# Kernel tuning notes

Measured on AMD Instinct MI355X. Metric: run time of the kernel, lower is better.

The kernel has to match this reference:

```python
import jax, jax.numpy as jnp
import numpy as np

DIM, HEADS, DHEAD = 256, 8, 64
INNER = HEADS * DHEAD
EPS = 1e-5


def _ln(x, g, b):
    m = x.mean(-1, keepdims=True)
    v = ((x - m) ** 2).mean(-1, keepdims=True)
    return (x - m) / jnp.sqrt(v + EPS) * g + b


def setup_inputs() -> dict:
    key = jax.random.key(0)
    ks = jax.random.split(key, 24)
    b, n, Q, K = 1, 6, 900, 1408
    d = DIM
    s = lambda fan_in: 1.0 / np.sqrt(fan_in)
    inp = {
        "k_g": jax.random.normal(ks[0], (b, n, K, d), jnp.float32),
        "q_g": jax.random.normal(ks[1], (b, n, Q, d), jnp.float32),
        "k_a": jax.random.normal(ks[2], (b, n, K, d), jnp.float32),
        "q_a": jax.random.normal(ks[3], (b, Q, d), jnp.float32),
        "v": jax.random.normal(ks[4], (b, n, K, d), jnp.float32),
        "mask": jax.random.randint(ks[5], (b, n, K), 0, 2).astype(bool),
        # projections (stored as (in, out))
        "W_qg": jax.random.uniform(ks[6], (d, INNER), jnp.float32, -s(d), s(d)),
        "b_qg": jnp.zeros((INNER,), jnp.float32),
        "W_kg": jax.random.uniform(ks[7], (d, INNER), jnp.float32, -s(d), s(d)),
        "b_kg": jnp.zeros((INNER,), jnp.float32),
        "W_qa": jax.random.uniform(ks[8], (d, INNER), jnp.float32, -s(d), s(d)),
        "b_qa": jnp.zeros((INNER,), jnp.float32),
        "W_ka": jax.random.uniform(ks[9], (d, INNER), jnp.float32, -s(d), s(d)),
        "b_ka": jnp.zeros((INNER,), jnp.float32),
        "W_v": jax.random.uniform(ks[10], (d, INNER), jnp.float32, -s(d), s(d)),
        "b_v": jnp.zeros((INNER,), jnp.float32),
        "W_o": jax.random.uniform(ks[11], (INNER, d), jnp.float32, -s(INNER), s(INNER)),
        "b_o": jnp.zeros((d,), jnp.float32),
        "ln1_g": jnp.ones((d,), jnp.float32),
        "ln1_b": jnp.zeros((d,), jnp.float32),
        "W_m1": jax.random.uniform(ks[12], (d, 2 * d), jnp.float32, -s(d), s(d)),
        "b_m1": jnp.zeros((2 * d,), jnp.float32),
        "W_m2": jax.random.uniform(ks[13], (2 * d, d), jnp.float32, -s(2 * d), s(2 * d)),
        "b_m2": jnp.zeros((d,), jnp.float32),
        "ln2_g": jnp.ones((d,), jnp.float32),
        "ln2_b": jnp.zeros((d,), jnp.float32),
        "scale_g": jnp.full((HEADS,), DHEAD ** -0.5, jnp.float32),
        "scale_a": jnp.full((HEADS,), DHEAD ** -0.5, jnp.float32),
    }
    return inp


def reference(k_g, q_g, k_a, q_a, v, mask,
              W_qg, b_qg, W_kg, b_kg, W_qa, b_qa, W_ka, b_ka, W_v, b_v,
              W_o, b_o, ln1_g, ln1_b, W_m1, b_m1, W_m2, b_m2, ln2_g, ln2_b,
              scale_g, scale_a):
    b, n, Q, _ = q_g.shape
    K = k_g.shape[2]
    h, dh = HEADS, DHEAD
    skip = q_a

    def split(x):  # (..., h*dh) -> (b, h, ..., dh)
        return jnp.moveaxis(x.reshape(x.shape[:-1] + (h, dh)), -2, 1)

    kg = split(k_g @ W_kg + b_kg)          # (b, h, n, K, dh)
    qg = split(q_g @ W_qg + b_qg)          # (b, h, n, Q, dh)
    ka = split(k_a @ W_ka + b_ka)          # (b, h, n, K, dh)
    qa = split(q_a @ W_qa + b_qa)          # (b, h, Q, dh)
    vv = split(v @ W_v + b_v)              # (b, h, n, K, dh)

    dot_g = jnp.einsum('bhnqd,bhnkd->bhnqk', qg, kg)
    dot_a = jnp.einsum('bhqd,bhnkd->bhnqk', qa, ka)
    sg = scale_g[None, :, None, None, None]
    sa = scale_a[None, :, None, None, None]
    dot = sg * dot_g + sa * dot_a
    dot = jnp.where(mask[:, None, :, None, :], -jnp.inf, dot)

    # softmax jointly over (n, K)
    dot = dot.transpose(0, 1, 3, 2, 4).reshape(b, h, Q, n * K)
    att = jax.nn.softmax(dot, axis=-1)
    vflat = vv.reshape(b, h, n * K, dh)
    a = jnp.einsum('bhqk,bhkd->bhqd', att, vflat)
    a = a.transpose(0, 2, 1, 3).reshape(b, Q, h * dh)

    z = a @ W_o + b_o + skip
    z = _ln(z, ln1_g, ln1_b)
    z = z + (jax.nn.gelu(z @ W_m1 + b_m1, approximate=False) @ W_m2 + b_m2)
    z = _ln(z, ln2_g, ln2_b)
    return z
```

## Files before the change

kernel.cpp:

```cpp
#include <hip/hip_runtime.h>
#include <stdint.h>

typedef unsigned short u16;
typedef _Float16 half8 __attribute__((ext_vector_type(8)));
typedef _Float16 half4 __attribute__((ext_vector_type(4)));
typedef _Float16 half2 __attribute__((ext_vector_type(2)));
typedef float f32x4 __attribute__((ext_vector_type(4)));

__device__ __forceinline__ u16 f2h(float f) {
    _Float16 h = (_Float16)f; u16 u; __builtin_memcpy(&u, &h, 2); return u;
}
__device__ __forceinline__ float h2f(u16 u) {
    _Float16 h; __builtin_memcpy(&h, &u, 2); return (float)h;
}

template<int CTRL>
__device__ __forceinline__ float dppf(float x) {
    return __builtin_bit_cast(float,
        __builtin_amdgcn_update_dpp(0, __builtin_bit_cast(int, x), CTRL, 0xF, 0xF, false));
}
__device__ __forceinline__ float sum16(float x) {
    x += dppf<0xB1>(x);
    x += dppf<0x4E>(x);
    x += dppf<0x124>(x);
    x += dppf<0x128>(x);
    return x;
}

__global__ __launch_bounds__(256) void prep_kernel(
    const float* __restrict__ W_qg, const float* __restrict__ W_kg,
    const float* __restrict__ W_qa, const float* __restrict__ W_ka,
    const float* __restrict__ W_v,  const float* __restrict__ W_o,
    const float* __restrict__ W_m1, const float* __restrict__ W_m2,
    u16* __restrict__ T_qg, u16* __restrict__ T_kg, u16* __restrict__ T_qa,
    u16* __restrict__ T_ka, u16* __restrict__ T_v,  u16* __restrict__ T_o,
    u16* __restrict__ T_m1, u16* __restrict__ T_m2,
    const float* __restrict__ scale_g, const float* __restrict__ scale_a,
    const float* __restrict__ b_kg, const float* __restrict__ b_ka,
    float* __restrict__ bkg_s, float* __restrict__ bka_s,
    const int* __restrict__ mask, int* __restrict__ mflag)
{
    const int z = blockIdx.z;
    const int tid = threadIdx.x;
    if (z == 8) {
        if (blockIdx.y != 0) return;
        if (blockIdx.x == 0) {
            __shared__ int f;
            if (tid == 0) f = 0;
            __syncthreads();
            int local = 0;
            for (int i = tid; i < 2112; i += 256) { int vv = mask[i]; if (vv & ~1) local = 1; }
            if (local) atomicOr(&f, 1);
            __syncthreads();
            if (tid == 0) *mflag = f;
        } else if (blockIdx.x == 1) {
            for (int j = tid; j < 512; j += 256) {
                bkg_s[j] = b_kg[j] * scale_g[j >> 6];
                bka_s[j] = b_ka[j] * scale_a[j >> 6];
            }
        }
        return;
    }
    const int K = (z == 5 || z == 7) ? 512 : 256;
    const int N = (z == 5 || z == 7) ? 256 : 512;
    const int k0 = blockIdx.x * 64, n0 = blockIdx.y * 64;
    if (k0 >= K || n0 >= N) return;
    const float* W = z==0?W_qg: z==1?W_kg: z==2?W_qa: z==3?W_ka: z==4?W_v: z==5?W_o: z==6?W_m1: W_m2;
    u16* D        = z==0?T_qg: z==1?T_kg: z==2?T_qa: z==3?T_ka: z==4?T_v: z==5?T_o: z==6?T_m1: T_m2;
    const float* scp = z==1 ? scale_g : z==3 ? scale_a : nullptr;

    __shared__ u16 T[64][80];
    const int cr = tid >> 4, cc = (tid & 15) * 4;
    const float sc = scp ? scp[(n0 + cc) >> 6] : 1.0f;
    #pragma unroll
    for (int i = 0; i < 4; ++i) {
        const int r = cr + i * 16;
        const float4 vv = *(const float4*)(W + (size_t)(k0 + r) * N + n0 + cc);
        T[cc + 0][r] = f2h(vv.x * sc);
        T[cc + 1][r] = f2h(vv.y * sc);
        T[cc + 2][r] = f2h(vv.z * sc);
        T[cc + 3][r] = f2h(vv.w * sc);
    }
    __syncthreads();
    const int nr = tid >> 2, part = (tid & 3) * 16;
    u16* drow = D + (size_t)(n0 + nr) * K + k0 + part;
    *(half8*)(drow)     = *(const half8*)&T[nr][part];
    *(half8*)(drow + 8) = *(const half8*)&T[nr][part + 8];
}

__global__ __launch_bounds__(256, 4) void proj_all(
    const float* __restrict__ k_g, const float* __restrict__ k_a,
    const float* __restrict__ v,   const float* __restrict__ q_g,
    const float* __restrict__ q_a,
    const u16* __restrict__ T_kg, const u16* __restrict__ T_ka,
    const u16* __restrict__ T_v,  const u16* __restrict__ T_qg,
    const u16* __restrict__ T_qa,
    const float* __restrict__ bkg_s, const float* __restrict__ bka_s,
    const float* __restrict__ b_v,   const float* __restrict__ b_qg,
    const float* __restrict__ b_qa,
    u16* __restrict__ qcat, u16* __restrict__ kcat, u16* __restrict__ vt)
{
    __shared__ u16 Ws[256 * 36];

    int bx = blockIdx.x;
    int mode, M;
    const float* X; const u16* Wt; const float* bias; u16* out;
    if (bx < 132)      { mode = 2; M = 8448; X = k_g; Wt = T_kg; bias = bkg_s; out = kcat; }
    else if (bx < 264) { mode = 3; M = 8448; X = k_a; Wt = T_ka; bias = bka_s; out = kcat; bx -= 132; }
    else if (bx < 396) { mode = 4; M = 8448; X = v;   Wt = T_v;  bias = b_v;   out = vt;   bx -= 264; }
    else if (bx < 481) { mode = 0; M = 5400; X = q_g; Wt = T_qg; bias = b_qg;  out = qcat; bx -= 396; }
    else               { mode = 1; M = 900;  X = q_a; Wt = T_qa; bias = b_qa;  out = qcat; bx -= 481; }
    const int rows_per_n = (mode == 0) ? 900 : 1408;

    const int tid = threadIdx.x;
    const int w = tid >> 6, lane = tid & 63;
    const int l15 = lane & 15, quad = lane >> 4;
    const int m0 = bx * 64;
    const int nbase = blockIdx.y * 256;
    const int row = m0 + w * 16 + l15;

    const float* xrow = X + (size_t)(row < M ? row : 0) * 256 + quad * 8;
    const u16* wcol = Wt + ((size_t)(nbase + tid) << 8);

    f32x4 o[4][4];
    #pragma unroll
    for (int nt = 0; nt < 4; ++nt)
        #pragma unroll
        for (int t = 0; t < 4; ++t) { o[nt][t][0]=0.f; o[nt][t][1]=0.f; o[nt][t][2]=0.f; o[nt][t][3]=0.f; }

    for (int k0 = 0; k0 < 8; ++k0) {
        {
            const uint4 w0 = *(const uint4*)(wcol + k0 * 32 + 0);
            const uint4 w1 = *(const uint4*)(wcol + k0 * 32 + 8);
            const uint4 w2 = *(const uint4*)(wcol + k0 * 32 + 16);
            const uint4 w3 = *(const uint4*)(wcol + k0 * 32 + 24);
            *(uint4*)&Ws[tid * 36 + 0]  = w0;
            *(uint4*)&Ws[tid * 36 + 8]  = w1;
            *(uint4*)&Ws[tid * 36 + 16] = w2;
            *(uint4*)&Ws[tid * 36 + 24] = w3;
        }
        __syncthreads();

        const float4 a0 = *(const float4*)(xrow + k0 * 32);
        const float4 a1 = *(const float4*)(xrow + k0 * 32 + 4);
        half8 af;
        af[0]=(_Float16)a0.x; af[1]=(_Float16)a0.y; af[2]=(_Float16)a0.z; af[3]=(_Float16)a0.w;
        af[4]=(_Float16)a1.x; af[5]=(_Float16)a1.y; af[6]=(_Float16)a1.z; af[7]=(_Float16)a1.w;

        #pragma unroll
        for (int nt = 0; nt < 4; ++nt)
            #pragma unroll
            for (int t = 0; t < 4; ++t) {
                const half8 bf = *(const half8*)&Ws[(nt * 64 + t * 16 + l15) * 36 + quad * 8];
                o[nt][t] = __builtin_amdgcn_mfma_f32_16x16x32_f16(af, bf, o[nt][t], 0, 0, 0);
            }
        __syncthreads();
    }

    #pragma unroll
    for (int nt = 0; nt < 4; ++nt) {
        const int n0 = nbase + nt * 64;
        const int hh = n0 >> 6;
        float bj[4];
        #pragma unroll
        for (int t = 0; t < 4; ++t) bj[t] = bias[n0 + t * 16 + l15];

        if (mode == 4) {
            const int gr0 = m0 + w * 16 + quad * 4;
            if (gr0 < M) {
                const int nI = gr0 / rows_per_n;
                const int rr = gr0 - nI * rows_per_n;
                u16* vb = out + (size_t)(hh * 6 + nI) * 64 * 1408;
                #pragma unroll
                for (int t = 0; t < 4; ++t) {
                    const int d = t * 16 + l15;
                    ushort4 pk;
                    pk.x = f2h(o[nt][t][0] + bj[t]);
                    pk.y = f2h(o[nt][t][1] + bj[t]);
                    pk.z = f2h(o[nt][t][2] + bj[t]);
                    pk.w = f2h(o[nt][t][3] + bj[t]);
                    *(ushort4*)&vb[(size_t)d * 1408 + rr] = pk;
                }
            }
        } else if (mode == 1) {
            #pragma unroll
            for (int r = 0; r < 4; ++r) {
                const int gr = m0 + w * 16 + quad * 4 + r;
                if (gr < M) {
                    for (int nb = 0; nb < 6; ++nb) {
                        u16* qb = out + (((size_t)(hh * 6 + nb) * 900 + gr) << 7) + 64;
                        #pragma unroll
                        for (int t = 0; t < 4; ++t)
                            qb[t * 16 + l15] = f2h(o[nt][t][r] + bj[t]);
                    }
                }
            }
        } else {
            const size_t kdim = (mode == 0) ? 900 : 1408;
            const int doff = (mode == 3) ? 64 : 0;
            #pragma unroll
            for (int r = 0; r < 4; ++r) {
                const int gr = m0 + w * 16 + quad * 4 + r;
                if (gr < M) {
                    const int nI = gr / rows_per_n;
                    const int rr = gr - nI * rows_per_n;
                    u16* ob = out + (((size_t)(hh * 6 + nI) * kdim + rr) << 7) + doff;
                    #pragma unroll
                    for (int t = 0; t < 4; ++t)
                        ob[t * 16 + l15] = f2h(o[nt][t][r] + bj[t]);
                }
            }
        }
    }
}

__global__ __launch_bounds__(512, 4) void attn_kernel(
    const u16* __restrict__ qcat, const u16* __restrict__ kcat,
    const u16* __restrict__ vt, const void* __restrict__ maskp,
    const int* __restrict__ mflag,
    u16* __restrict__ Opart, float* __restrict__ lpart)
{
    __shared__ __align__(16) u16 Ks[64 * 136];
    __shared__ __align__(16) u16 Vs[64 * 72];
    __shared__ __align__(16) u16 Ps[8][1216];
    __shared__ float Mb[64];

    const int flat = blockIdx.x;
    const int hn_i = (flat & 7) + 8 * ((flat >> 3) % 6);
    const int rest = flat / 48;
    const int qt = rest & 7;
    const int sp = rest >> 3;
    const int n = hn_i - (hn_i / 6) * 6;

    const int q0 = qt * 128;
    const int tid = threadIdx.x;
    const int w = tid >> 6, lane = tid & 63;
    const int l15 = lane & 15, quad = lane >> 4;
    const bool m8 = (*mflag != 0);
    const size_t hn = (size_t)hn_i;

    const u16* kbase = kcat + ((hn * 1408) << 7);
    const u16* vbase = vt + hn * 64 * 1408;
    const unsigned char* mB = (const unsigned char*)maskp;
    const int* mI = (const int*)maskp;
    const int mko = n * 1408;

    const int krow_s = tid >> 4;
    const int kcol_s = (tid & 15) * 8;
    const int vrow_s = tid >> 3;
    const int vcol_s = (tid & 7) * 8;

    half8 qf[4];
    {
        const int gq = q0 + w * 16 + l15;
        if (gq < 900) {
            const u16* qrow = qcat + ((hn * 900 + gq) << 7) + quad * 8;
            #pragma unroll
            for (int k0 = 0; k0 < 4; ++k0)
                qf[k0] = *(const half8*)(qrow + k0 * 32);
        } else {
            #pragma unroll
            for (int k0 = 0; k0 < 4; ++k0)
                #pragma unroll
                for (int j = 0; j < 8; ++j) qf[k0][j] = (_Float16)0.0f;
        }
    }

    half8 onesb;
    {
        const _Float16 ov = (l15 == 0) ? (_Float16)1.0f : (_Float16)0.0f;
        #pragma unroll
        for (int j = 0; j < 8; ++j) onesb[j] = ov;
    }

    f32x4 o[4];
    f32x4 l16;
    #pragma unroll
    for (int t = 0; t < 4; ++t) { o[t][0]=0.f; o[t][1]=0.f; o[t][2]=0.f; o[t][3]=0.f; }
    l16[0]=0.f; l16[1]=0.f; l16[2]=0.f; l16[3]=0.f;

    uint4 kA, kB, vA;
    float mreg = 0.0f;
    {
        const int k0c = sp * 11 * 64;
        kA = *(const uint4*)(kbase + ((size_t)(k0c +  0 + krow_s) << 7) + kcol_s);
        kB = *(const uint4*)(kbase + ((size_t)(k0c + 32 + krow_s) << 7) + kcol_s);
        vA = *(const uint4*)(vbase + (size_t)(vrow_s) * 1408 + k0c + vcol_s);
        if (tid < 64) {
            const int ki = mko + k0c + tid;
            const int mv = m8 ? (int)mB[ki] : mI[ki];
            mreg = mv ? -1e30f : 0.0f;
        }
    }

    for (int cc = 0; cc < 11; ++cc) {
        *(uint4*)&Ks[( 0 + krow_s) * 136 + kcol_s] = kA;
        *(uint4*)&Ks[(32 + krow_s) * 136 + kcol_s] = kB;
        *(uint4*)&Vs[vrow_s * 72 + vcol_s] = vA;
        if (tid < 64) Mb[tid] = mreg;
        __syncthreads();

        if (cc < 10) {
            const int k0n = (sp * 11 + cc + 1) * 64;
            kA = *(const uint4*)(kbase + ((size_t)(k0n +  0 + krow_s) << 7) + kcol_s);
            kB = *(const uint4*)(kbase + ((size_t)(k0n + 32 + krow_s) << 7) + kcol_s);
            vA = *(const uint4*)(vbase + (size_t)(vrow_s) * 1408 + k0n + vcol_s);
            if (tid < 64) {
                const int ki = mko + k0n + tid;
                const int mv = m8 ? (int)mB[ki] : mI[ki];
                mreg = mv ? -1e30f : 0.0f;
            }
        }

        f32x4 s[4];
        #pragma unroll
        for (int t = 0; t < 4; ++t) {
            const float mbv = Mb[t * 16 + l15];
            s[t][0]=mbv; s[t][1]=mbv; s[t][2]=mbv; s[t][3]=mbv;
        }
        #pragma unroll
        for (int k0 = 0; k0 < 4; ++k0)
            #pragma unroll
            for (int t = 0; t < 4; ++t) {
                const half8 kf = *(const half8*)&Ks[(t * 16 + l15) * 136 + k0 * 32 + quad * 8];
                s[t] = __builtin_amdgcn_mfma_f32_16x16x32_f16(qf[k0], kf, s[t], 0, 0, 0);
            }

        #pragma unroll
        for (int r = 0; r < 4; ++r) {
            const float p0 = __expf(s[0][r]);
            const float p1 = __expf(s[1][r]);
            const float p2 = __expf(s[2][r]);
            const float p3 = __expf(s[3][r]);
            u16* pr = &Ps[w][(quad * 4 + r) * 72 + quad * 16 + l15];
            pr[0]  = f2h(p0);
            pr[16] = f2h(p1);
            pr[32] = f2h(p2);
            pr[48] = f2h(p3);
        }

        const u16* prow = &Ps[w][l15 * 72 + (l15 >> 2) * 16 + quad * 8];
        const half8 pa0 = *(const half8*)(prow);
        const half8 pa1 = *(const half8*)(prow + 32);

        l16 = __builtin_amdgcn_mfma_f32_16x16x32_f16(pa0, onesb, l16, 0, 0, 0);
        l16 = __builtin_amdgcn_mfma_f32_16x16x32_f16(pa1, onesb, l16, 0, 0, 0);

        #pragma unroll
        for (int t = 0; t < 4; ++t) {
            const half8 v0 = *(const half8*)&Vs[(t * 16 + l15) * 72 + quad * 8];
            const half8 v1 = *(const half8*)&Vs[(t * 16 + l15) * 72 + 32 + quad * 8];
            o[t] = __builtin_amdgcn_mfma_f32_16x16x32_f16(pa0, v0, o[t], 0, 0, 0);
            o[t] = __builtin_amdgcn_mfma_f32_16x16x32_f16(pa1, v1, o[t], 0, 0, 0);
        }
        __syncthreads();
    }

    const int p = sp * 48 + hn_i;
    #pragma unroll
    for (int r = 0; r < 4; ++r) {
        const int gq = q0 + w * 16 + quad * 4 + r;
        if (gq < 900) {
            u16* db = Opart + ((size_t)p * 900 + gq) * 64 + l15;
            db[0]  = f2h(o[0][r]);
            db[16] = f2h(o[1][r]);
            db[32] = f2h(o[2][r]);
            db[48] = f2h(o[3][r]);
            if (l15 == 0) lpart[p * 900 + gq] = l16[r];
        }
    }
}

__global__ __launch_bounds__(256) void epi_mega(
    const u16* __restrict__ Opart, const float* __restrict__ lpart,
    const u16* __restrict__ T_o,
    const u16* __restrict__ T_m1, const u16* __restrict__ T_m2,
    const float* __restrict__ b_o, const float* __restrict__ q_a,
    const float* __restrict__ ln1_g, const float* __restrict__ ln1_b,
    const float* __restrict__ b_m1, const float* __restrict__ b_m2,
    const float* __restrict__ ln2_g, const float* __restrict__ ln2_b,
    float* __restrict__ outf)
{
    __shared__ u16 A16[2][520];
    __shared__ u16 Z1[16][264];
    __shared__ u16 H[16][520];
    __shared__ float Ssum[4][16];
    __shared__ float Ssq[4][16];

    const int tid = threadIdx.x;
    const int w = tid >> 6, lane = tid & 63;
    const int l15 = lane & 15, quad = lane >> 4;
    const int m0 = blockIdx.x * 2;

    {
        const int r = tid >> 7;
        const int cg = tid & 127;
        const int c4 = cg * 4;
        const int hh = cg >> 4;
        const int d4 = (cg & 15) * 4;
        const int q = m0 + r;
        float l = 0.f;
        float a0 = 0.f, a1 = 0.f, a2 = 0.f, a3 = 0.f;
        #pragma unroll
        for (int s = 0; s < 12; ++s) {
            const int p = ((s & 1) ? 48 : 0) + hh * 6 + (s >> 1);
            l += lpart[p * 900 + q];
            const ushort4 t0 = *(const ushort4*)&Opart[((size_t)p * 900 + q) * 64 + d4];
            a0 += h2f(t0.x); a1 += h2f(t0.y); a2 += h2f(t0.z); a3 += h2f(t0.w);
        }
        const float inv = 1.0f / fmaxf(l, 1e-30f);
        ushort4 o0;
        o0.x = f2h(a0 * inv); o0.y = f2h(a1 * inv); o0.z = f2h(a2 * inv); o0.w = f2h(a3 * inv);
        *(ushort4*)&A16[r][c4] = o0;
    }
    __syncthreads();

    {
        f32x4 acc[4];
        #pragma unroll
        for (int t = 0; t < 4; ++t) { acc[t][0]=0.f; acc[t][1]=0.f; acc[t][2]=0.f; acc[t][3]=0.f; }

        #pragma unroll
        for (int k0 = 0; k0 < 16; ++k0) {
            const half8 af = *(const half8*)&A16[l15 & 1][k0 * 32 + quad * 8];
            #pragma unroll
            for (int t = 0; t < 4; ++t) {
                const int nn = w * 64 + t * 16 + l15;
                const half8 bf = *(const half8*)(T_o + (size_t)nn * 512 + k0 * 32 + quad * 8);
                acc[t] = __builtin_amdgcn_mfma_f32_16x16x32_f16(af, bf, acc[t], 0, 0, 0);
            }
        }

        float vals[4][4];
        #pragma unroll
        for (int r = 0; r < 4; ++r) {
            const int row = m0 + ((quad * 4 + r) & 1);
            float s = 0.f, sq = 0.f;
            #pragma unroll
            for (int t = 0; t < 4; ++t) {
                const int col = w * 64 + t * 16 + l15;
                const float x = acc[t][r] + b_o[col] + q_a[(size_t)row * 256 + col];
                vals[r][t] = x; s += x; sq += x * x;
            }
            s = sum16(s); sq = sum16(sq);
            if (l15 == 0) { Ssum[w][quad * 4 + r] = s; Ssq[w][quad * 4 + r] = sq; }
        }
        __syncthreads();

        #pragma unroll
        for (int r = 0; r < 4; ++r) {
            const int rl = quad * 4 + r;
            const float st = Ssum[0][rl] + Ssum[1][rl] + Ssum[2][rl] + Ssum[3][rl];
            const float qt = Ssq[0][rl] + Ssq[1][rl] + Ssq[2][rl] + Ssq[3][rl];
            const float mean = st * (1.0f / 256.0f);
            const float var  = qt * (1.0f / 256.0f) - mean * mean;
            const float inv  = rsqrtf(var + 1e-5f);
            #pragma unroll
            for (int t = 0; t < 4; ++t) {
                const int col = w * 64 + t * 16 + l15;
                const float z = (vals[r][t] - mean) * inv * ln1_g[col] + ln1_b[col];
                Z1[rl][col] = f2h(z);
            }
        }
        __syncthreads();
    }

    {
        f32x4 acc[8];
        #pragma unroll
        for (int t = 0; t < 8; ++t) { acc[t][0]=0.f; acc[t][1]=0.f; acc[t][2]=0.f; acc[t][3]=0.f; }

        #pragma unroll
        for (int k0 = 0; k0 < 8; ++k0) {
            const half8 af = *(const half8*)&Z1[l15][k0 * 32 + quad * 8];
            #pragma unroll
            for (int t = 0; t < 8; ++t) {
                const int nn = w * 128 + t * 16 + l15;
                const half8 bf = *(const half8*)(T_m1 + (size_t)nn * 256 + k0 * 32 + quad * 8);
                acc[t] = __builtin_amdgcn_mfma_f32_16x16x32_f16(af, bf, acc[t], 0, 0, 0);
            }
        }

        #pragma unroll
        for (int r = 0; r < 4; ++r) {
            const int rl = quad * 4 + r;
            #pragma unroll
            for (int t = 0; t < 8; ++t) {
                const int col = w * 128 + t * 16 + l15;
                const float x = acc[t][r] + b_m1[col];
                H[rl][col] = f2h(0.5f * x * (1.0f + erff(x * 0.70710678118654752f)));
            }
        }
        __syncthreads();
    }

    {
        f32x4 acc[4];
        #pragma unroll
        for (int t = 0; t < 4; ++t) { acc[t][0]=0.f; acc[t][1]=0.f; acc[t][2]=0.f; acc[t][3]=0.f; }

        #pragma unroll
        for (int k0 = 0; k0 < 16; ++k0) {
            const half8 af = *(const half8*)&H[l15][k0 * 32 + quad * 8];
            #pragma unroll
            for (int t = 0; t < 4; ++t) {
                const int nn = w * 64 + t * 16 + l15;
                const half8 bf = *(const half8*)(T_m2 + (size_t)nn * 512 + k0 * 32 + quad * 8);
                acc[t] = __builtin_amdgcn_mfma_f32_16x16x32_f16(af, bf, acc[t], 0, 0, 0);
            }
        }

        float vals[4][4];
        #pragma unroll
        for (int r = 0; r < 4; ++r) {
            const int rl = quad * 4 + r;
            float s = 0.f, sq = 0.f;
            #pragma unroll
            for (int t = 0; t < 4; ++t) {
                const int col = w * 64 + t * 16 + l15;
                const float x = acc[t][r] + b_m2[col] + h2f(Z1[rl][col]);
                vals[r][t] = x; s += x; sq += x * x;
            }
            s = sum16(s); sq = sum16(sq);
            if (l15 == 0) { Ssum[w][rl] = s; Ssq[w][rl] = sq; }
        }
        __syncthreads();

        #pragma unroll
        for (int r = 0; r < 4; ++r) {
            const int rl = quad * 4 + r;
            const float st = Ssum[0][rl] + Ssum[1][rl] + Ssum[2][rl] + Ssum[3][rl];
            const float qt = Ssq[0][rl] + Ssq[1][rl] + Ssq[2][rl] + Ssq[3][rl];
            const float mean = st * (1.0f / 256.0f);
            const float var  = qt * (1.0f / 256.0f) - mean * mean;
            const float inv  = rsqrtf(var + 1e-5f);
            const int row = m0 + rl;
            if (rl < 2 && row < 900) {
                #pragma unroll
                for (int t = 0; t < 4; ++t) {
                    const int col = w * 64 + t * 16 + l15;
                    outf[(size_t)row * 256 + col] = (vals[r][t] - mean) * inv * ln2_g[col] + ln2_b[col];
                }
            }
        }
    }
}

extern "C" void kernel_launch(void* const* d_in, const int* in_sizes, int n_in,
                              void* d_out, int out_size, void* d_ws, size_t ws_size,
                              hipStream_t stream)
{
    const float* k_g  = (const float*)d_in[0];
    const float* q_g  = (const float*)d_in[1];
    const float* k_a  = (const float*)d_in[2];
    const float* q_a  = (const float*)d_in[3];
    const float* v    = (const float*)d_in[4];
    const void*  mask = d_in[5];
    const float* W_qg = (const float*)d_in[6];
    const float* b_qg = (const float*)d_in[7];
    const float* W_kg = (const float*)d_in[8];
    const float* b_kg = (const float*)d_in[9];
    const float* W_qa = (const float*)d_in[10];
    const float* b_qa = (const float*)d_in[11];
    const float* W_ka = (const float*)d_in[12];
    const float* b_ka = (const float*)d_in[13];
    const float* W_v  = (const float*)d_in[14];
    const float* b_v  = (const float*)d_in[15];
    const float* W_o  = (const float*)d_in[16];
    const float* b_o  = (const float*)d_in[17];
    const float* ln1_g = (const float*)d_in[18];
    const float* ln1_b = (const float*)d_in[19];
    const float* W_m1 = (const float*)d_in[20];
    const float* b_m1 = (const float*)d_in[21];
    const float* W_m2 = (const float*)d_in[22];
    const float* b_m2 = (const float*)d_in[23];
    const float* ln2_g = (const float*)d_in[24];
    const float* ln2_b = (const float*)d_in[25];
    const float* scale_g = (const float*)d_in[26];
    const float* scale_a = (const float*)d_in[27];

    char* ws = (char*)d_ws;
    size_t off = 0;
    auto alloc = [&](size_t bytes) -> void* {
        void* p = ws + off;
        off += (bytes + 255) & ~(size_t)255;
        return p;
    };
    u16*   qcat  = (u16*)  alloc((size_t)8 * 6 * 900  * 128 * 2);
    u16*   kcat  = (u16*)  alloc((size_t)8 * 6 * 1408 * 128 * 2);
    u16*   vt    = (u16*)  alloc((size_t)8 * 6 * 64 * 1408 * 2);
    u16*   Tw[8];
    for (int i = 0; i < 8; ++i) Tw[i] = (u16*)alloc((size_t)512 * 256 * 2);
    float* bkg_s = (float*)alloc((size_t)512 * 4);
    float* bka_s = (float*)alloc((size_t)512 * 4);
    int*   mflag = (int*)  alloc(256);
    u16*   Opart = (u16*)  alloc((size_t)96 * 900 * 64 * 2);
    float* lpart = (float*)alloc((size_t)96 * 900 * 4);

    prep_kernel<<<dim3(8, 8, 9), 256, 0, stream>>>(
        W_qg, W_kg, W_qa, W_ka, W_v, W_o, W_m1, W_m2,
        Tw[0], Tw[1], Tw[2], Tw[3], Tw[4], Tw[5], Tw[6], Tw[7],
        scale_g, scale_a, b_kg, b_ka, bkg_s, bka_s, (const int*)mask, mflag);

    proj_all<<<dim3(496, 2), 256, 0, stream>>>(
        k_g, k_a, v, q_g, q_a,
        Tw[1], Tw[3], Tw[4], Tw[0], Tw[2],
        bkg_s, bka_s, b_v, b_qg, b_qa,
        qcat, kcat, vt);

    attn_kernel<<<768, 512, 0, stream>>>(qcat, kcat, vt, mask, mflag, Opart, lpart);

    epi_mega<<<450, 256, 0, stream>>>(
        Opart, lpart, Tw[5], Tw[6], Tw[7],
        b_o, q_a, ln1_g, ln1_b, b_m1, b_m2, ln2_g, ln2_b,
        (float*)d_out);
}
```

Baseline: 252.2 us.

## Process four query rows per epilogue block with split-K across two wave groups

The fused epilogue now handles four query rows per block instead of two and runs 512 threads. The eight waves split the K dimension of each of the three GEMMs (W_o, W_m1, W_m2) into two halves, and the partial accumulators are summed through a new 32KB LDS buffer. This halves the number of blocks, so each weight tile streamed from global memory is reused across twice as many rows. The cost is extra LDS traffic and barriers for the reduction, plus larger per-block LDS use that may lower occupancy.

```diff
diff --git a/kernel.cpp b/kernel.cpp
--- a/kernel.cpp
+++ b/kernel.cpp
@@ -371,7 +371,7 @@
     }
 }
 
-__global__ __launch_bounds__(256) void epi_mega(
+__global__ __launch_bounds__(512) void epi_mega(
     const u16* __restrict__ Opart, const float* __restrict__ lpart,
     const u16* __restrict__ T_o,
     const u16* __restrict__ T_m1, const u16* __restrict__ T_m2,
@@ -381,16 +381,19 @@
     const float* __restrict__ ln2_g, const float* __restrict__ ln2_b,
     float* __restrict__ outf)
 {
-    __shared__ u16 A16[2][520];
+    __shared__ u16 A16[4][520];
     __shared__ u16 Z1[16][264];
     __shared__ u16 H[16][520];
+    __shared__ float Red[256 * 32];
     __shared__ float Ssum[4][16];
     __shared__ float Ssq[4][16];
 
     const int tid = threadIdx.x;
     const int w = tid >> 6, lane = tid & 63;
+    const int w4 = w & 3, kh = w >> 2;
+    const int t256 = tid & 255;
     const int l15 = lane & 15, quad = lane >> 4;
-    const int m0 = blockIdx.x * 2;
+    const int m0 = blockIdx.x * 4;
 
     {
         const int r = tid >> 7;
@@ -420,46 +423,66 @@
         #pragma unroll
         for (int t = 0; t < 4; ++t) { acc[t][0]=0.f; acc[t][1]=0.f; acc[t][2]=0.f; acc[t][3]=0.f; }
 
-        #pragma unroll
-        for (int k0 = 0; k0 < 16; ++k0) {
-            const half8 af = *(const half8*)&A16[l15 & 1][k0 * 32 + quad * 8];
+        const int kbase = kh * 8;
+        #pragma unroll
+        for (int kk = 0; kk < 8; ++kk) {
+            const int k0 = kbase + kk;
+            const half8 af = *(const half8*)&A16[l15 & 3][k0 * 32 + quad * 8];
             #pragma unroll
             for (int t = 0; t < 4; ++t) {
-                const int nn = w * 64 + t * 16 + l15;
+                const int nn = w4 * 64 + t * 16 + l15;
                 const half8 bf = *(const half8*)(T_o + (size_t)nn * 512 + k0 * 32 + quad * 8);
                 acc[t] = __builtin_amdgcn_mfma_f32_16x16x32_f16(af, bf, acc[t], 0, 0, 0);
             }
         }
 
+        if (kh == 1) {
+            #pragma unroll
+            for (int t = 0; t < 4; ++t)
+                #pragma unroll
+                for (int r = 0; r < 4; ++r)
+                    Red[t256 * 16 + t * 4 + r] = acc[t][r];
+        }
+        __syncthreads();
+        if (kh == 0) {
+            #pragma unroll
+            for (int t = 0; t < 4; ++t)
+                #pragma unroll
+                for (int r = 0; r < 4; ++r)
+                    acc[t][r] += Red[t256 * 16 + t * 4 + r];
+        }
+
         float vals[4][4];
         #pragma unroll
         for (int r = 0; r < 4; ++r) {
-            const int row = m0 + ((quad * 4 + r) & 1);
+            const int row = m0 + ((quad * 4 + r) & 3);
             float s = 0.f, sq = 0.f;
             #pragma unroll
             for (int t = 0; t < 4; ++t) {
-                const int col = w * 64 + t * 16 + l15;
+                const int col = w4 * 64 + t * 16 + l15;
                 const float x = acc[t][r] + b_o[col] + q_a[(size_t)row * 256 + col];
                 vals[r][t] = x; s += x; sq += x * x;
             }
             s = sum16(s); sq = sum16(sq);
-            if (l15 == 0) { Ssum[w][quad * 4 + r] = s; Ssq[w][quad * 4 + r] = sq; }
-        }
-        __syncthreads();
-
-        #pragma unroll
-        for (int r = 0; r < 4; ++r) {
-            const int rl = quad * 4 + r;
-            const float st = Ssum[0][rl] + Ssum[1][rl] + Ssum[2][rl] + Ssum[3][rl];
-            const float qt = Ssq[0][rl] + Ssq[1][rl] + Ssq[2][rl] + Ssq[3][rl];
-            const float mean = st * (1.0f / 256.0f);
-            const float var  = qt * (1.0f / 256.0f) - mean * mean;
-            const float inv  = rsqrtf(var + 1e-5f);
-            #pragma unroll
-            for (int t = 0; t < 4; ++t) {
-                const int col = w * 64 + t * 16 + l15;
-                const float z = (vals[r][t] - mean) * inv * ln1_g[col] + ln1_b[col];
-                Z1[rl][col] = f2h(z);
+            if (l15 == 0 && kh == 0) { Ssum[w4][quad * 4 + r] = s; Ssq[w4][quad * 4 + r] = sq; }
+        }
+        __syncthreads();
+
+        if (kh == 0) {
+            #pragma unroll
+            for (int r = 0; r < 4; ++r) {
+                const int rl = quad * 4 + r;
+                const float st = Ssum[0][rl] + Ssum[1][rl] + Ssum[2][rl] + Ssum[3][rl];
+                const float qt = Ssq[0][rl] + Ssq[1][rl] + Ssq[2][rl] + Ssq[3][rl];
+                const float mean = st * (1.0f / 256.0f);
+                const float var  = qt * (1.0f / 256.0f) - mean * mean;
+                const float inv  = rsqrtf(var + 1e-5f);
+                #pragma unroll
+                for (int t = 0; t < 4; ++t) {
+                    const int col = w4 * 64 + t * 16 + l15;
+                    const float z = (vals[r][t] - mean) * inv * ln1_g[col] + ln1_b[col];
+                    Z1[rl][col] = f2h(z);
+                }
             }
         }
         __syncthreads();
@@ -470,25 +493,37 @@
         #pragma unroll
         for (int t = 0; t < 8; ++t) { acc[t][0]=0.f; acc[t][1]=0.f; acc[t][2]=0.f; acc[t][3]=0.f; }
 
-        #pragma unroll
-        for (int k0 = 0; k0 < 8; ++k0) {
+        const int kbase = kh * 4;
+        #pragma unroll
+        for (int kk = 0; kk < 4; ++kk) {
+            const int k0 = kbase + kk;
             const half8 af = *(const half8*)&Z1[l15][k0 * 32 + quad * 8];
             #pragma unroll
             for (int t = 0; t < 8; ++t) {
-                const int nn = w * 128 + t * 16 + l15;
+                const int nn = w4 * 128 + t * 16 + l15;
                 const half8 bf = *(const half8*)(T_m1 + (size_t)nn * 256 + k0 * 32 + quad * 8);
                 acc[t] = __builtin_amdgcn_mfma_f32_16x16x32_f16(af, bf, acc[t], 0, 0, 0);
             }
         }
 
-        #pragma unroll
-        for (int r = 0; r < 4; ++r) {
-            const int rl = quad * 4 + r;
-            #pragma unroll
-            for (int t = 0; t < 8; ++t) {
-                const int col = w * 128 + t * 16 + l15;
-                const float x = acc[t][r] + b_m1[col];
-                H[rl][col] = f2h(0.5f * x * (1.0f + erff(x * 0.70710678118654752f)));
+        if (kh == 1) {
+            #pragma unroll
+            for (int t = 0; t < 8; ++t)
+                #pragma unroll
+                for (int r = 0; r < 4; ++r)
+                    Red[t256 * 32 + t * 4 + r] = acc[t][r];
+        }
+        __syncthreads();
+        if (kh == 0) {
+            #pragma unroll
+            for (int r = 0; r < 4; ++r) {
+                const int rl = quad * 4 + r;
+                #pragma unroll
+                for (int t = 0; t < 8; ++t) {
+                    const int col = w4 * 128 + t * 16 + l15;
+                    const float x = acc[t][r] + Red[t256 * 32 + t * 4 + r] + b_m1[col];
+                    H[rl][col] = f2h(0.5f * x * (1.0f + erff(x * 0.70710678118654752f)));
+                }
             }
         }
         __syncthreads();
@@ -499,15 +534,33 @@
         #pragma unroll
         for (int t = 0; t < 4; ++t) { acc[t][0]=0.f; acc[t][1]=0.f; acc[t][2]=0.f; acc[t][3]=0.f; }
 
-        #pragma unroll
-        for (int k0 = 0; k0 < 16; ++k0) {
+        const int kbase = kh * 8;
+        #pragma unroll
+        for (int kk = 0; kk < 8; ++kk) {
+            const int k0 = kbase + kk;
             const half8 af = *(const half8*)&H[l15][k0 * 32 + quad * 8];
             #pragma unroll
             for (int t = 0; t < 4; ++t) {
-                const int nn = w * 64 + t * 16 + l15;
+                const int nn = w4 * 64 + t * 16 + l15;
                 const half8 bf = *(const half8*)(T_m2 + (size_t)nn * 512 + k0 * 32 + quad * 8);
                 acc[t] = __builtin_amdgcn_mfma_f32_16x16x32_f16(af, bf, acc[t], 0, 0, 0);
             }
+        }
+
+        if (kh == 1) {
+            #pragma unroll
+            for (int t = 0; t < 4; ++t)
+                #pragma unroll
+                for (int r = 0; r < 4; ++r)
+                    Red[t256 * 16 + t * 4 + r] = acc[t][r];
+        }
+        __syncthreads();
+        if (kh == 0) {
+            #pragma unroll
+            for (int t = 0; t < 4; ++t)
+                #pragma unroll
+                for (int r = 0; r < 4; ++r)
+                    acc[t][r] += Red[t256 * 16 + t * 4 + r];
         }
 
         float vals[4][4];
@@ -517,29 +570,31 @@
             float s = 0.f, sq = 0.f;
             #pragma unroll
             for (int t = 0; t < 4; ++t) {
-                const int col = w * 64 + t * 16 + l15;
-                const float x = acc[t][r] + b_m2[col] + h2f(Z1[rl][col]);
+                const int col = w4 * 64 + t * 16 + l15;
+                const float x = acc[t][r] + b_m2[col] + h2f(Z1[rl & 3][col]);
                 vals[r][t] = x; s += x; sq += x * x;
             }
             s = sum16(s); sq = sum16(sq);
-            if (l15 == 0) { Ssum[w][rl] = s; Ssq[w][rl] = sq; }
-        }
-        __syncthreads();
-
-        #pragma unroll
-        for (int r = 0; r < 4; ++r) {
-            const int rl = quad * 4 + r;
-            const float st = Ssum[0][rl] + Ssum[1][rl] + Ssum[2][rl] + Ssum[3][rl];
-            const float qt = Ssq[0][rl] + Ssq[1][rl] + Ssq[2][rl] + Ssq[3][rl];
-            const float mean = st * (1.0f / 256.0f);
-            const float var  = qt * (1.0f / 256.0f) - mean * mean;
-            const float inv  = rsqrtf(var + 1e-5f);
-            const int row = m0 + rl;
-            if (rl < 2 && row < 900) {
-                #pragma unroll
-                for (int t = 0; t < 4; ++t) {
-                    const int col = w * 64 + t * 16 + l15;
-                    outf[(size_t)row * 256 + col] = (vals[r][t] - mean) * inv * ln2_g[col] + ln2_b[col];
+            if (l15 == 0 && kh == 0) { Ssum[w4][rl] = s; Ssq[w4][rl] = sq; }
+        }
+        __syncthreads();
+
+        if (kh == 0) {
+            #pragma unroll
+            for (int r = 0; r < 4; ++r) {
+                const int rl = quad * 4 + r;
+                const float st = Ssum[0][rl] + Ssum[1][rl] + Ssum[2][rl] + Ssum[3][rl];
+                const float qt = Ssq[0][rl] + Ssq[1][rl] + Ssq[2][rl] + Ssq[3][rl];
+                const float mean = st * (1.0f / 256.0f);
+                const float var  = qt * (1.0f / 256.0f) - mean * mean;
+                const float inv  = rsqrtf(var + 1e-5f);
+                const int row = m0 + rl;
+                if (rl < 4 && row < 900) {
+                    #pragma unroll
+                    for (int t = 0; t < 4; ++t) {
+                        const int col = w4 * 64 + t * 16 + l15;
+                        outf[(size_t)row * 256 + col] = (vals[r][t] - mean) * inv * ln2_g[col] + ln2_b[col];
+                    }
                 }
             }
         }
@@ -610,7 +665,7 @@
 
     attn_kernel<<<768, 512, 0, stream>>>(qcat, kcat, vt, mask, mflag, Opart, lpart);
 
-    epi_mega<<<450, 256, 0, stream>>>(
+    epi_mega<<<225, 512, 0, stream>>>(
         Opart, lpart, Tw[5], Tw[6], Tw[7],
         b_o, q_a, ln1_g, ln1_b, b_m1, b_m2, ln2_g, ln2_b,
         (float*)d_out);
```

New measurement: 243.9 us. -3.3%, faster.
